# Kernel optimization log

Hardware: AMD Instinct MI355X
Metric: run time of the kernel (lower is better)

The kernel has to match this reference:

```python
import jax, jax.numpy as jnp
import numpy as np

NUM_ENT = 50000
N = 4 * NUM_ENT          # concat of id/gender/age/level embeds along dim 0
D = 128                  # init_dim = gcn_dim = embed_dim
H = 4                    # k_kernel attention heads
E = 600000
NUM_REL = 10
B = 4096


def _seg_softmax(scores, seg, n):
    # scores: [E, H], softmax over edges sharing the same destination node
    m = jax.ops.segment_max(scores, seg, num_segments=n)
    m = jnp.where(jnp.isfinite(m), m, 0.0)
    e = jnp.exp(scores - m[seg])
    s = jax.ops.segment_sum(e, seg, num_segments=n)
    return e / (s[seg] + 1e-16)


def _rgat_conv(x, rel_emb, src, dst, edge_type, W, W_rel, att):
    # CompGCN-style relational message (x_src + r_et) @ W, GAT-style attention,
    # per-destination segment softmax, scatter-sum aggregate, tanh activation.
    n = x.shape[0]
    xW = x @ W                        # [N, D_out]
    rW = rel_emb @ W                  # relation embed in message space
    d_out = xW.shape[1]
    dh = d_out // H
    m = (xW[src] + rW[edge_type]).reshape(-1, H, dh)   # [E, H, dh] messages
    q = xW[dst].reshape(-1, H, dh)                     # [E, H, dh] dest feats
    score = jax.nn.leaky_relu(
        (q * att[:, :dh]).sum(-1) + (m * att[:, dh:]).sum(-1), 0.2)  # [E, H]
    alpha = _seg_softmax(score, dst, n)                # [E, H]
    out = jax.ops.segment_sum((alpha[..., None] * m).reshape(-1, d_out), dst,
                              num_segments=n)          # [N, D_out]
    return jnp.tanh(out), rel_emb @ W_rel


def setup_inputs() -> dict:
    key = jax.random.key(0)
    ks = jax.random.split(key, 16)
    s = 0.1  # weight scale for numerical sanity
    return {
        "sub": jax.random.randint(ks[0], (B,), 0, N),
        "rel": jax.random.randint(ks[1], (B,), 0, 2 * NUM_REL),
        "edge_index": jax.random.randint(ks[2], (2, E), 0, N),
        "edge_type": jax.random.randint(ks[3], (E,), 0, 2 * NUM_REL),
        "ent_feature": jax.random.randint(ks[4], (NUM_ENT, 3), 0, 8),
        "gender_weight": s * jax.random.normal(ks[5], (8, D), jnp.float32),
        "age_weight": s * jax.random.normal(ks[6], (8, D), jnp.float32),
        "level_weight": s * jax.random.normal(ks[7], (8, D), jnp.float32),
        "id_embed": s * jax.random.normal(ks[8], (NUM_ENT, D), jnp.float32),
        "init_rel": s * jax.random.normal(ks[9], (2 * NUM_REL, D), jnp.float32),
        "W1": s * jax.random.normal(ks[10], (D, D), jnp.float32),
        "Wr1": s * jax.random.normal(ks[11], (D, D), jnp.float32),
        "att1": s * jax.random.normal(ks[12], (H, 2 * (D // H)), jnp.float32),
        "W2": s * jax.random.normal(ks[13], (D, D), jnp.float32),
        "Wr2": s * jax.random.normal(ks[14], (D, D), jnp.float32),
        "att2": s * jax.random.normal(ks[15], (H, 2 * (D // H)), jnp.float32),
    }


def reference(sub, rel, edge_index, edge_type, ent_feature,
              gender_weight, age_weight, level_weight, id_embed, init_rel,
              W1, Wr1, att1, W2, Wr2, att2):
    # feature embedding gathers + concat along node axis (as in __init__)
    gender_embed = gender_weight[ent_feature[:, 0]]
    age_embed = age_weight[ent_feature[:, 1]]
    level_embed = level_weight[ent_feature[:, 2]]
    x = jnp.concatenate([id_embed, gender_embed, age_embed, level_embed], axis=0)  # [N, D]
    src, dst = edge_index[0], edge_index[1]
    r = init_rel
    x, r = _rgat_conv(x, r, src, dst, edge_type, W1, Wr1, att1)
    # dropout modules run as identity (eval mode)
    x, r = _rgat_conv(x, r, src, dst, edge_type, W2, Wr2, att2)
    sub_emb = x[sub]
    rel_emb = r[rel]
    return (sub_emb, rel_emb, x)
```

## Files before the change

kernel.cpp:

```cpp
#include <hip/hip_runtime.h>

#define D 128
#define HEADS 4

typedef __attribute__((ext_vector_type(8))) short short8;
typedef __attribute__((ext_vector_type(4))) float f32x4;

__device__ __forceinline__ short f2b(float f) {
    unsigned u = __float_as_uint(f);
    unsigned r = (u + 0x7FFFu + ((u >> 16) & 1u)) >> 16;
    return (short)r;
}

__global__ __launch_bounds__(256) void gemm_mfma(
    const unsigned short* __restrict__ Ab, const short* __restrict__ Wt,
    unsigned short* __restrict__ C, const float* __restrict__ att,
    float* __restrict__ ns, int buildmode,
    const int* __restrict__ ent_feature, const float* __restrict__ gw,
    const float* __restrict__ aw, const float* __restrict__ lw,
    const float* __restrict__ idemb, int num_ent)
{
    __shared__ short sA[64 * D];
    __shared__ short sW[D * D];

    const int t = threadIdx.x;
    const long row0 = (long)blockIdx.x * 64;

    {
        int srow = t >> 2;
        int q = t & 3;
        long grow = row0 + srow;
        if (buildmode == 2) {
            const short8* p8 = (const short8*)(Ab + grow * D);
            #pragma unroll
            for (int jb = 0; jb < 4; ++jb) {
                short8 blk = p8[q * 4 + jb];
                int kb = (q * 4 + jb) ^ (srow & 7);
                *(short8*)&sA[srow * D + kb * 8] = blk;
            }
        } else {
            const float* srcp;
            if (grow < num_ent)               srcp = idemb + grow * D;
            else if (grow < 2L * num_ent)     srcp = gw + (long)ent_feature[(grow - num_ent) * 3 + 0] * D;
            else if (grow < 3L * num_ent)     srcp = aw + (long)ent_feature[(grow - 2L * num_ent) * 3 + 1] * D;
            else                              srcp = lw + (long)ent_feature[(grow - 3L * num_ent) * 3 + 2] * D;
            const float4* p4 = (const float4*)srcp + q * 8;
            float v[32];
            #pragma unroll
            for (int j = 0; j < 8; ++j) {
                float4 f = p4[j];
                v[j * 4 + 0] = f.x; v[j * 4 + 1] = f.y; v[j * 4 + 2] = f.z; v[j * 4 + 3] = f.w;
            }
            #pragma unroll
            for (int jb = 0; jb < 4; ++jb) {
                short8 blk;
                #pragma unroll
                for (int e = 0; e < 8; ++e) blk[e] = f2b(v[jb * 8 + e]);
                int kb = (q * 4 + jb) ^ (srow & 7);
                *(short8*)&sA[srow * D + kb * 8] = blk;
            }
        }
    }

    {
        #pragma unroll
        for (int i = 0; i < 8; ++i) {
            int c = t + 256 * i;
            int row = c >> 4, kb = c & 15;
            short8 blk = *(const short8*)(Wt + c * 8);
            *(short8*)&sW[row * D + (kb ^ (row & 7)) * 8] = blk;
        }
    }
    __syncthreads();

    const int wv = t >> 6, lane = t & 63;
    const int cl = lane & 15, kg = lane >> 4;

    short8 a[4];
    #pragma unroll
    for (int ks = 0; ks < 4; ++ks)
        a[ks] = *(const short8*)&sA[(wv * 16 + cl) * D + (((ks * 4 + kg) ^ (cl & 7)) * 8)];

    f32x4 acc[8];
    #pragma unroll
    for (int ct = 0; ct < 8; ++ct) acc[ct] = (f32x4){0.f, 0.f, 0.f, 0.f};

    #pragma unroll
    for (int ct = 0; ct < 8; ++ct) {
        #pragma unroll
        for (int ks = 0; ks < 4; ++ks) {
            short8 b = *(const short8*)&sW[(ct * 16 + cl) * D + (((ks * 4 + kg) ^ (cl & 7)) * 8)];
            acc[ct] = __builtin_amdgcn_mfma_f32_16x16x32_bf16(a[ks], b, acc[ct], 0, 0, 0);
        }
    }

    unsigned short* Cp = C + (row0 + wv * 16 + kg * 4) * D;
    #pragma unroll
    for (int ct = 0; ct < 8; ++ct)
        #pragma unroll
        for (int j = 0; j < 4; ++j)
            Cp[j * D + ct * 16 + cl] = (unsigned short)f2b(acc[ct][j]);

    float aqc[8], amc[8];
    #pragma unroll
    for (int ct = 0; ct < 8; ++ct) {
        int h = ct >> 1, cc = (ct & 1) * 16 + cl;
        aqc[ct] = att[h * 64 + cc];
        amc[ct] = att[h * 64 + 32 + cc];
    }
    float* scr = (float*)sA + wv * 1024;
    #pragma unroll
    for (int pass = 0; pass < 2; ++pass) {
        __syncthreads();
        #pragma unroll
        for (int jj = 0; jj < 2; ++jj) {
            int j = pass * 2 + jj;
            f32x4 lo, hi;
            #pragma unroll
            for (int h = 0; h < 4; ++h) {
                float qv = acc[2 * h][j] * aqc[2 * h] + acc[2 * h + 1][j] * aqc[2 * h + 1];
                float sv = acc[2 * h][j] * amc[2 * h] + acc[2 * h + 1][j] * amc[2 * h + 1];
                if (h < 2) { lo[h * 2] = qv; lo[h * 2 + 1] = sv; }
                else       { hi[(h - 2) * 2] = qv; hi[(h - 2) * 2 + 1] = sv; }
            }
            int base = ((kg * 16 + cl) * 2 + jj) * 8;
            *(f32x4*)&scr[base] = lo;
            *(f32x4*)&scr[base + 4] = hi;
        }
        __syncthreads();
        int kgr = lane >> 4, rem = lane & 15;
        int jjr = rem >> 3, hr = (rem >> 1) & 3, tr = rem & 1;
        float ssum = 0.f;
        #pragma unroll
        for (int c = 0; c < 16; ++c)
            ssum += scr[((kgr * 16 + c) * 2 + jjr) * 8 + hr * 2 + tr];
        long rown = row0 + wv * 16 + kgr * 4 + pass * 2 + jjr;
        ns[rown * 8 + tr * 4 + hr] = ssum;
    }
}

__global__ void prep1(const float* __restrict__ init_rel,
                      const float* __restrict__ W1, const float* __restrict__ Wr1,
                      const float* __restrict__ W2, const float* __restrict__ att1,
                      float* __restrict__ rWb, float* __restrict__ r1,
                      float* __restrict__ srt,
                      short* __restrict__ Wt1, short* __restrict__ Wt2, int nrel)
{
    __shared__ float red[128];
    int b = blockIdx.x, c = threadIdx.x;
    if (b >= 2 * nrel) {
        int bb = b - 2 * nrel;
        const float* W = (bb < D) ? W1 : W2;
        short* Wt = (bb < D) ? Wt1 : Wt2;
        int n = bb & (D - 1);
        Wt[n * D + c] = f2b(W[c * D + n]);
        return;
    }
    int r = (b < nrel) ? b : b - nrel;
    const float* W = (b < nrel) ? W1 : Wr1;
    float* out = (b < nrel) ? rWb : r1;
    float s = 0.f;
    for (int k = 0; k < D; ++k) s = fmaf(init_rel[r * D + k], W[k * D + c], s);
    out[r * D + c] = s;
    if (b < nrel) {
        int h = c >> 5;
        red[c] = s * att1[h * 64 + 32 + (c & 31)];
        __syncthreads();
        if (c < 4) {
            float ss = 0.f;
            #pragma unroll
            for (int k = 0; k < 32; ++k) ss += red[c * 32 + k];
            srt[r * 4 + c] = ss;
        }
    }
}

__global__ void prep2(const float* __restrict__ r1,
                      const float* __restrict__ W2, const float* __restrict__ Wr2,
                      const float* __restrict__ att2,
                      float* __restrict__ rWb, float* __restrict__ r2,
                      float* __restrict__ srt, int nrel)
{
    __shared__ float red[128];
    int b = blockIdx.x, c = threadIdx.x;
    int r = (b < nrel) ? b : b - nrel;
    const float* W = (b < nrel) ? W2 : Wr2;
    float* out = (b < nrel) ? rWb : r2;
    float s = 0.f;
    for (int k = 0; k < D; ++k) s = fmaf(r1[r * D + k], W[k * D + c], s);
    out[r * D + c] = s;
    if (b < nrel) {
        int h = c >> 5;
        red[c] = s * att2[h * 64 + 32 + (c & 31)];
        __syncthreads();
        if (c < 4) {
            float ss = 0.f;
            #pragma unroll
            for (int k = 0; k < 32; ++k) ss += red[c * 32 + k];
            srt[r * 4 + c] = ss;
        }
    }
}

__global__ __launch_bounds__(256) void hist_deg(const int* __restrict__ dst,
                                                int* __restrict__ deg, int E_)
{
    int i = blockIdx.x * 256 + threadIdx.x;
    if (i < E_) atomicAdd(&deg[dst[i]], 1);
}

__global__ __launch_bounds__(256) void scan_local(const int* __restrict__ deg,
                                                  int* __restrict__ offs,
                                                  int* __restrict__ partial, int n)
{
    __shared__ int lds[256];
    int b = blockIdx.x, t = threadIdx.x;
    int base = b * 1024;
    int v[4]; int s = 0;
    #pragma unroll
    for (int j = 0; j < 4; ++j) {
        int idx = base + t * 4 + j;
        v[j] = idx < n ? deg[idx] : 0;
        s += v[j];
    }
    lds[t] = s;
    __syncthreads();
    int mysum = s;
    for (int off = 1; off < 256; off <<= 1) {
        int o = t >= off ? lds[t - off] : 0;
        __syncthreads();
        lds[t] += o;
        __syncthreads();
    }
    int excl = lds[t] - mysum;
    if (t == 255) partial[b] = lds[255];
    int run = excl;
    #pragma unroll
    for (int j = 0; j < 4; ++j) {
        int idx = base + t * 4 + j;
        if (idx < n) offs[idx] = run;
        run += v[j];
    }
}

__global__ void scan_partials(int* __restrict__ partial, int nb, int* __restrict__ offs, int n)
{
    if (threadIdx.x == 0 && blockIdx.x == 0) {
        int run = 0;
        for (int i = 0; i < nb; ++i) { int v = partial[i]; partial[i] = run; run += v; }
        offs[n] = run;
    }
}

__global__ __launch_bounds__(256) void scan_add(int* __restrict__ offs,
                                                const int* __restrict__ partial, int n)
{
    int idx = blockIdx.x * 256 + threadIdx.x;
    if (idx < n) offs[idx] += partial[idx >> 10];
}

__global__ __launch_bounds__(256) void scatter_edges(
    const int* __restrict__ src, const int* __restrict__ dst, const int* __restrict__ etype,
    const int* __restrict__ offs, int* __restrict__ deg,
    int* __restrict__ sorted, int E_)
{
    int i = blockIdx.x * 256 + threadIdx.x;
    if (i >= E_) return;
    int d = dst[i];
    int pos = offs[d] + atomicSub(&deg[d], 1) - 1;
    sorted[pos] = src[i] | (etype[i] << 18);
}

#define GATHER_SLOT(mb, sv, rv, sr, p, cond)                              \
    unsigned mb = 0; float sv = 0.f, sr = 0.f; float2 rv = {0.f, 0.f};    \
    if (cond) { int s_ = (p) & 0x3FFFF, t_ = (p) >> 18;                   \
        mb = *(const unsigned*)(xWb + (long)s_ * D + 2 * lane);           \
        sv = ns[(long)s_ * 8 + 4 + h];                                    \
        rv = *(const float2*)(rW + (long)t_ * D + 2 * lane);              \
        sr = srt[t_ * 4 + h]; }

#define ACCUM_SLOT(mb, sv, rv, sr, qd, srun, ax, ay, cond)                \
    if (cond) { float mx = __uint_as_float(mb << 16) + rv.x;              \
        float my = __uint_as_float(mb & 0xFFFF0000u) + rv.y;              \
        float sc = qd + sv + sr; sc = sc > 0.f ? sc : 0.2f * sc;          \
        float we = __expf(sc);                                            \
        srun += we; ax = fmaf(we, mx, ax); ay = fmaf(we, my, ay); }

__global__ __launch_bounds__(256) void agg_node(
    const int* __restrict__ offs, const int* __restrict__ sedge,
    const unsigned short* __restrict__ xWb, const float* __restrict__ rW,
    const float* __restrict__ ns, const float* __restrict__ srt,
    void* __restrict__ outx, int out_bf16, int Nn)
{
    int wid = threadIdx.x >> 6;
    int lane = threadIdx.x & 63;
    long nA = (long)blockIdx.x * 8 + wid * 2;
    if (nA >= Nn) return;
    bool hasB = (nA + 1 < Nn);
    int h = lane >> 4;

    float qdA = ns[nA * 8 + h];
    float qdB = hasB ? ns[(nA + 1) * 8 + h] : 0.f;

    int2 oA = *(const int2*)&offs[nA];
    int e0A = oA.x, e1A = oA.y;
    int e0B = e1A, e1B = hasB ? offs[nA + 2] : e1A;

    float srunA = 0.f, axA = 0.f, ayA = 0.f;
    float srunB = 0.f, axB = 0.f, ayB = 0.f;

    int iA = e0A, iB = e0B;
    while (iA < e1A || iB < e1B) {
        int pA0 = (iA     < e1A) ? sedge[iA]     : 0;
        int pA1 = (iA + 1 < e1A) ? sedge[iA + 1] : 0;
        int pA2 = (iA + 2 < e1A) ? sedge[iA + 2] : 0;
        int pA3 = (iA + 3 < e1A) ? sedge[iA + 3] : 0;
        int pB0 = (iB     < e1B) ? sedge[iB]     : 0;
        int pB1 = (iB + 1 < e1B) ? sedge[iB + 1] : 0;
        int pB2 = (iB + 2 < e1B) ? sedge[iB + 2] : 0;
        int pB3 = (iB + 3 < e1B) ? sedge[iB + 3] : 0;

        GATHER_SLOT(mA0, vA0, rA0, sA0, pA0, iA     < e1A)
        GATHER_SLOT(mA1, vA1, rA1, sA1, pA1, iA + 1 < e1A)
        GATHER_SLOT(mA2, vA2, rA2, sA2, pA2, iA + 2 < e1A)
        GATHER_SLOT(mA3, vA3, rA3, sA3, pA3, iA + 3 < e1A)
        GATHER_SLOT(mB0, vB0, rB0, sB0, pB0, iB     < e1B)
        GATHER_SLOT(mB1, vB1, rB1, sB1, pB1, iB + 1 < e1B)
        GATHER_SLOT(mB2, vB2, rB2, sB2, pB2, iB + 2 < e1B)
        GATHER_SLOT(mB3, vB3, rB3, sB3, pB3, iB + 3 < e1B)

        ACCUM_SLOT(mA0, vA0, rA0, sA0, qdA, srunA, axA, ayA, iA     < e1A)
        ACCUM_SLOT(mA1, vA1, rA1, sA1, qdA, srunA, axA, ayA, iA + 1 < e1A)
        ACCUM_SLOT(mA2, vA2, rA2, sA2, qdA, srunA, axA, ayA, iA + 2 < e1A)
        ACCUM_SLOT(mA3, vA3, rA3, sA3, qdA, srunA, axA, ayA, iA + 3 < e1A)
        ACCUM_SLOT(mB0, vB0, rB0, sB0, qdB, srunB, axB, ayB, iB     < e1B)
        ACCUM_SLOT(mB1, vB1, rB1, sB1, qdB, srunB, axB, ayB, iB + 1 < e1B)
        ACCUM_SLOT(mB2, vB2, rB2, sB2, qdB, srunB, axB, ayB, iB + 2 < e1B)
        ACCUM_SLOT(mB3, vB3, rB3, sB3, qdB, srunB, axB, ayB, iB + 3 < e1B)

        iA += 4; iB += 4;
    }

    {
        float inv = 1.0f / (srunA + 1e-16f);
        float ox = tanhf(axA * inv);
        float oy = tanhf(ayA * inv);
        if (out_bf16) {
            unsigned pk = ((unsigned)(unsigned short)f2b(oy) << 16) | (unsigned short)f2b(ox);
            *(unsigned*)((unsigned short*)outx + nA * D + 2 * lane) = pk;
        } else {
            float2 o; o.x = ox; o.y = oy;
            *(float2*)((float*)outx + nA * D + 2 * lane) = o;
        }
    }
    if (hasB) {
        float inv = 1.0f / (srunB + 1e-16f);
        float ox = tanhf(axB * inv);
        float oy = tanhf(ayB * inv);
        if (out_bf16) {
            unsigned pk = ((unsigned)(unsigned short)f2b(oy) << 16) | (unsigned short)f2b(ox);
            *(unsigned*)((unsigned short*)outx + (nA + 1) * D + 2 * lane) = pk;
        } else {
            float2 o; o.x = ox; o.y = oy;
            *(float2*)((float*)outx + (nA + 1) * D + 2 * lane) = o;
        }
    }
}

__global__ void gather_out(const int* __restrict__ sub, const int* __restrict__ rel,
                           const float* __restrict__ xsrc, const float* __restrict__ rsrc,
                           float* __restrict__ out_sub, float* __restrict__ out_rel, int b)
{
    long i = (long)blockIdx.x * 256 + threadIdx.x;
    long tot = (long)b * 32;
    if (i < tot) {
        long row = i >> 5; int q = (int)(i & 31);
        ((float4*)out_sub)[i] = ((const float4*)(xsrc + (long)sub[row] * D))[q];
    } else if (i < 2 * tot) {
        long j = i - tot;
        long row = j >> 5; int q = (int)(j & 31);
        ((float4*)out_rel)[j] = ((const float4*)(rsrc + (long)rel[row] * D))[q];
    }
}

extern "C" void kernel_launch(void* const* d_in, const int* in_sizes, int n_in,
                              void* d_out, int out_size, void* d_ws, size_t ws_size,
                              hipStream_t stream)
{
    const int*   sub        = (const int*)d_in[0];
    const int*   rel        = (const int*)d_in[1];
    const int*   edge_index = (const int*)d_in[2];
    const int*   edge_type  = (const int*)d_in[3];
    const int*   ent_feat   = (const int*)d_in[4];
    const float* gw         = (const float*)d_in[5];
    const float* aw         = (const float*)d_in[6];
    const float* lw         = (const float*)d_in[7];
    const float* idemb      = (const float*)d_in[8];
    const float* init_rel   = (const float*)d_in[9];
    const float* W1         = (const float*)d_in[10];
    const float* Wr1        = (const float*)d_in[11];
    const float* att1       = (const float*)d_in[12];
    const float* W2         = (const float*)d_in[13];
    const float* Wr2        = (const float*)d_in[14];
    const float* att2       = (const float*)d_in[15];

    const int  Bn      = in_sizes[0];
    const int  E_      = in_sizes[3];
    const int  num_ent = in_sizes[4] / 3;
    const long Nn      = 4L * num_ent;
    const int  nrel    = in_sizes[9] / D;

    const int* srcp = edge_index;
    const int* dstp = edge_index + E_;

    float* out_sub = (float*)d_out;
    float* out_rel = out_sub + (long)Bn * D;
    float* out_x   = out_rel + (long)Bn * D;

    unsigned short* xWb = (unsigned short*)d_ws;
    unsigned short* x1b = xWb + Nn * D;
    int*   offs   = (int*)(x1b + Nn * D);
    int*   deg    = offs + (Nn + 1);
    int*   sorted = deg + Nn;
    int*   partial= sorted + E_;
    float* rWb    = (float*)(partial + 1024);
    float* r1     = rWb + (long)nrel * D;
    float* r2     = r1 + (long)nrel * D;
    short* Wt1    = (short*)(r2 + (long)nrel * D);
    short* Wt2    = Wt1 + D * D;
    float* ns     = (float*)(Wt2 + D * D);
    float* srt    = ns + Nn * 8;

    dim3 blk(256);
    int gemm_blocks  = (int)(Nn / 64);
    int e_blocks     = (E_ + 255) / 256;
    int agg_blocks   = (int)((Nn + 7) / 8);
    int gat_blocks   = (int)((2L * Bn * 32 + 255) / 256);
    int scan_blocks  = (int)((Nn + 1023) / 1024);
    int sadd_blocks  = (int)((Nn + 255) / 256);

    prep1<<<2 * nrel + 256, D, 0, stream>>>(init_rel, W1, Wr1, W2, att1,
                                            rWb, r1, srt, Wt1, Wt2, nrel);

    hipMemsetAsync(deg, 0, Nn * sizeof(int), stream);
    hist_deg<<<e_blocks, blk, 0, stream>>>(dstp, deg, E_);
    scan_local<<<scan_blocks, blk, 0, stream>>>(deg, offs, partial, (int)Nn);
    scan_partials<<<1, 64, 0, stream>>>(partial, scan_blocks, offs, (int)Nn);
    scan_add<<<sadd_blocks, blk, 0, stream>>>(offs, partial, (int)Nn);
    scatter_edges<<<e_blocks, blk, 0, stream>>>(srcp, dstp, edge_type, offs, deg, sorted, E_);

    gemm_mfma<<<gemm_blocks, blk, 0, stream>>>(nullptr, Wt1, xWb, att1, ns, 1,
                                               ent_feat, gw, aw, lw, idemb, num_ent);
    agg_node<<<agg_blocks, blk, 0, stream>>>(offs, sorted, xWb, rWb, ns, srt, x1b, 1, (int)Nn);

    prep2<<<2 * nrel, D, 0, stream>>>(r1, W2, Wr2, att2, rWb, r2, srt, nrel);
    gemm_mfma<<<gemm_blocks, blk, 0, stream>>>(x1b, Wt2, xWb, att2, ns, 2,
                                               nullptr, nullptr, nullptr, nullptr, nullptr, num_ent);
    agg_node<<<agg_blocks, blk, 0, stream>>>(offs, sorted, xWb, rWb, ns, srt, out_x, 0, (int)Nn);

    gather_out<<<gat_blocks, blk, 0, stream>>>(sub, rel, out_x, r2, out_sub, out_rel, Bn);
}
```

Measured before the change: 306.8 us.

## Store relation messages as bf16 and simplify aggregation to one node per wave

The per-relation message table rW is now stored as bf16 instead of fp32. Edges are packed as (src<<8)|etype so gather addresses come from byte offsets with fewer index multiplies. The aggregation kernel drops the two-nodes-per-wave interleave and processes one node per wave with 4-edge unrolling, launching twice as many blocks. This cuts per-edge load bytes and address arithmetic, but gives up the extra memory-level parallelism of interleaving two nodes and rounds relation embeddings to bf16.

```diff
diff --git a/kernel.cpp b/kernel.cpp
--- a/kernel.cpp
+++ b/kernel.cpp
@@ -142,7 +142,7 @@
 __global__ void prep1(const float* __restrict__ init_rel,
                       const float* __restrict__ W1, const float* __restrict__ Wr1,
                       const float* __restrict__ W2, const float* __restrict__ att1,
-                      float* __restrict__ rWb, float* __restrict__ r1,
+                      unsigned short* __restrict__ rw16, float* __restrict__ r1,
                       float* __restrict__ srt,
                       short* __restrict__ Wt1, short* __restrict__ Wt2, int nrel)
 {
@@ -158,11 +158,10 @@
     }
     int r = (b < nrel) ? b : b - nrel;
     const float* W = (b < nrel) ? W1 : Wr1;
-    float* out = (b < nrel) ? rWb : r1;
     float s = 0.f;
     for (int k = 0; k < D; ++k) s = fmaf(init_rel[r * D + k], W[k * D + c], s);
-    out[r * D + c] = s;
     if (b < nrel) {
+        rw16[r * D + c] = (unsigned short)f2b(s);
         int h = c >> 5;
         red[c] = s * att1[h * 64 + 32 + (c & 31)];
         __syncthreads();
@@ -172,24 +171,25 @@
             for (int k = 0; k < 32; ++k) ss += red[c * 32 + k];
             srt[r * 4 + c] = ss;
         }
+    } else {
+        r1[r * D + c] = s;
     }
 }
 
 __global__ void prep2(const float* __restrict__ r1,
                       const float* __restrict__ W2, const float* __restrict__ Wr2,
                       const float* __restrict__ att2,
-                      float* __restrict__ rWb, float* __restrict__ r2,
+                      unsigned short* __restrict__ rw16, float* __restrict__ r2,
                       float* __restrict__ srt, int nrel)
 {
     __shared__ float red[128];
     int b = blockIdx.x, c = threadIdx.x;
     int r = (b < nrel) ? b : b - nrel;
     const float* W = (b < nrel) ? W2 : Wr2;
-    float* out = (b < nrel) ? rWb : r2;
     float s = 0.f;
     for (int k = 0; k < D; ++k) s = fmaf(r1[r * D + k], W[k * D + c], s);
-    out[r * D + c] = s;
     if (b < nrel) {
+        rw16[r * D + c] = (unsigned short)f2b(s);
         int h = c >> 5;
         red[c] = s * att2[h * 64 + 32 + (c & 31)];
         __syncthreads();
@@ -199,6 +199,8 @@
             for (int k = 0; k < 32; ++k) ss += red[c * 32 + k];
             srt[r * 4 + c] = ss;
         }
+    } else {
+        r2[r * D + c] = s;
     }
 }
 
@@ -262,108 +264,81 @@
 __global__ __launch_bounds__(256) void scatter_edges(
     const int* __restrict__ src, const int* __restrict__ dst, const int* __restrict__ etype,
     const int* __restrict__ offs, int* __restrict__ deg,
-    int* __restrict__ sorted, int E_)
+    unsigned* __restrict__ sorted, int E_)
 {
     int i = blockIdx.x * 256 + threadIdx.x;
     if (i >= E_) return;
     int d = dst[i];
     int pos = offs[d] + atomicSub(&deg[d], 1) - 1;
-    sorted[pos] = src[i] | (etype[i] << 18);
-}
-
-#define GATHER_SLOT(mb, sv, rv, sr, p, cond)                              \
-    unsigned mb = 0; float sv = 0.f, sr = 0.f; float2 rv = {0.f, 0.f};    \
-    if (cond) { int s_ = (p) & 0x3FFFF, t_ = (p) >> 18;                   \
-        mb = *(const unsigned*)(xWb + (long)s_ * D + 2 * lane);           \
-        sv = ns[(long)s_ * 8 + 4 + h];                                    \
-        rv = *(const float2*)(rW + (long)t_ * D + 2 * lane);              \
-        sr = srt[t_ * 4 + h]; }
-
-#define ACCUM_SLOT(mb, sv, rv, sr, qd, srun, ax, ay, cond)                \
-    if (cond) { float mx = __uint_as_float(mb << 16) + rv.x;              \
-        float my = __uint_as_float(mb & 0xFFFF0000u) + rv.y;              \
-        float sc = qd + sv + sr; sc = sc > 0.f ? sc : 0.2f * sc;          \
-        float we = __expf(sc);                                            \
+    sorted[pos] = ((unsigned)src[i] << 8) | (unsigned)etype[i];
+}
+
+#define GATHER_SLOT(mb, sv, rv, sr, p, cond)                                 \
+    unsigned mb = 0, rv = 0; float sv = 0.f, sr = 0.f;                       \
+    if (cond) { unsigned rowb = (p) & 0xFFFFFF00u;                           \
+        unsigned etb = ((p) & 0xFFu) << 8;                                   \
+        mb = *(const unsigned*)(xb + rowb + lo4);                            \
+        sv = *(const float*)(nb + (rowb >> 3) + ho4);                        \
+        rv = *(const unsigned*)(rb + etb + lo4);                             \
+        sr = *(const float*)(sb + (etb >> 4) + (ho4 - 16)); }
+
+#define ACCUM_SLOT(mb, sv, rv, sr, cond)                                     \
+    if (cond) {                                                              \
+        float mx = __uint_as_float(mb << 16) + __uint_as_float(rv << 16);    \
+        float my = __uint_as_float(mb & 0xFFFF0000u) + __uint_as_float(rv & 0xFFFF0000u); \
+        float sc = qd + sv + sr; sc = sc > 0.f ? sc : 0.2f * sc;             \
+        float we = __expf(sc);                                               \
         srun += we; ax = fmaf(we, mx, ax); ay = fmaf(we, my, ay); }
 
 __global__ __launch_bounds__(256) void agg_node(
-    const int* __restrict__ offs, const int* __restrict__ sedge,
-    const unsigned short* __restrict__ xWb, const float* __restrict__ rW,
+    const int* __restrict__ offs, const unsigned* __restrict__ sedge,
+    const unsigned short* __restrict__ xWb, const unsigned short* __restrict__ rw16,
     const float* __restrict__ ns, const float* __restrict__ srt,
     void* __restrict__ outx, int out_bf16, int Nn)
 {
     int wid = threadIdx.x >> 6;
     int lane = threadIdx.x & 63;
-    long nA = (long)blockIdx.x * 8 + wid * 2;
-    if (nA >= Nn) return;
-    bool hasB = (nA + 1 < Nn);
+    long node = (long)blockIdx.x * 4 + wid;
+    if (node >= Nn) return;
     int h = lane >> 4;
 
-    float qdA = ns[nA * 8 + h];
-    float qdB = hasB ? ns[(nA + 1) * 8 + h] : 0.f;
-
-    int2 oA = *(const int2*)&offs[nA];
-    int e0A = oA.x, e1A = oA.y;
-    int e0B = e1A, e1B = hasB ? offs[nA + 2] : e1A;
-
-    float srunA = 0.f, axA = 0.f, ayA = 0.f;
-    float srunB = 0.f, axB = 0.f, ayB = 0.f;
-
-    int iA = e0A, iB = e0B;
-    while (iA < e1A || iB < e1B) {
-        int pA0 = (iA     < e1A) ? sedge[iA]     : 0;
-        int pA1 = (iA + 1 < e1A) ? sedge[iA + 1] : 0;
-        int pA2 = (iA + 2 < e1A) ? sedge[iA + 2] : 0;
-        int pA3 = (iA + 3 < e1A) ? sedge[iA + 3] : 0;
-        int pB0 = (iB     < e1B) ? sedge[iB]     : 0;
-        int pB1 = (iB + 1 < e1B) ? sedge[iB + 1] : 0;
-        int pB2 = (iB + 2 < e1B) ? sedge[iB + 2] : 0;
-        int pB3 = (iB + 3 < e1B) ? sedge[iB + 3] : 0;
-
-        GATHER_SLOT(mA0, vA0, rA0, sA0, pA0, iA     < e1A)
-        GATHER_SLOT(mA1, vA1, rA1, sA1, pA1, iA + 1 < e1A)
-        GATHER_SLOT(mA2, vA2, rA2, sA2, pA2, iA + 2 < e1A)
-        GATHER_SLOT(mA3, vA3, rA3, sA3, pA3, iA + 3 < e1A)
-        GATHER_SLOT(mB0, vB0, rB0, sB0, pB0, iB     < e1B)
-        GATHER_SLOT(mB1, vB1, rB1, sB1, pB1, iB + 1 < e1B)
-        GATHER_SLOT(mB2, vB2, rB2, sB2, pB2, iB + 2 < e1B)
-        GATHER_SLOT(mB3, vB3, rB3, sB3, pB3, iB + 3 < e1B)
-
-        ACCUM_SLOT(mA0, vA0, rA0, sA0, qdA, srunA, axA, ayA, iA     < e1A)
-        ACCUM_SLOT(mA1, vA1, rA1, sA1, qdA, srunA, axA, ayA, iA + 1 < e1A)
-        ACCUM_SLOT(mA2, vA2, rA2, sA2, qdA, srunA, axA, ayA, iA + 2 < e1A)
-        ACCUM_SLOT(mA3, vA3, rA3, sA3, qdA, srunA, axA, ayA, iA + 3 < e1A)
-        ACCUM_SLOT(mB0, vB0, rB0, sB0, qdB, srunB, axB, ayB, iB     < e1B)
-        ACCUM_SLOT(mB1, vB1, rB1, sB1, qdB, srunB, axB, ayB, iB + 1 < e1B)
-        ACCUM_SLOT(mB2, vB2, rB2, sB2, qdB, srunB, axB, ayB, iB + 2 < e1B)
-        ACCUM_SLOT(mB3, vB3, rB3, sB3, qdB, srunB, axB, ayB, iB + 3 < e1B)
-
-        iA += 4; iB += 4;
-    }
-
-    {
-        float inv = 1.0f / (srunA + 1e-16f);
-        float ox = tanhf(axA * inv);
-        float oy = tanhf(ayA * inv);
-        if (out_bf16) {
-            unsigned pk = ((unsigned)(unsigned short)f2b(oy) << 16) | (unsigned short)f2b(ox);
-            *(unsigned*)((unsigned short*)outx + nA * D + 2 * lane) = pk;
-        } else {
-            float2 o; o.x = ox; o.y = oy;
-            *(float2*)((float*)outx + nA * D + 2 * lane) = o;
-        }
-    }
-    if (hasB) {
-        float inv = 1.0f / (srunB + 1e-16f);
-        float ox = tanhf(axB * inv);
-        float oy = tanhf(ayB * inv);
-        if (out_bf16) {
-            unsigned pk = ((unsigned)(unsigned short)f2b(oy) << 16) | (unsigned short)f2b(ox);
-            *(unsigned*)((unsigned short*)outx + (nA + 1) * D + 2 * lane) = pk;
-        } else {
-            float2 o; o.x = ox; o.y = oy;
-            *(float2*)((float*)outx + (nA + 1) * D + 2 * lane) = o;
-        }
+    const char* xb = (const char*)xWb;
+    const char* rb = (const char*)rw16;
+    const char* nb = (const char*)ns;
+    const char* sb = (const char*)srt;
+    const int lo4 = 4 * lane;
+    const int ho4 = 16 + 4 * h;
+
+    float qd = ns[node * 8 + h];
+    int e0 = offs[node], e1 = offs[node + 1];
+    float srun = 0.f, ax = 0.f, ay = 0.f;
+
+    for (int base = e0; base < e1; base += 4) {
+        unsigned p0 = sedge[base];
+        unsigned p1 = (base + 1 < e1) ? sedge[base + 1] : 0;
+        unsigned p2 = (base + 2 < e1) ? sedge[base + 2] : 0;
+        unsigned p3 = (base + 3 < e1) ? sedge[base + 3] : 0;
+
+        GATHER_SLOT(m0, v0, r0, s0, p0, true)
+        GATHER_SLOT(m1, v1, r1, s1, p1, base + 1 < e1)
+        GATHER_SLOT(m2, v2, r2, s2, p2, base + 2 < e1)
+        GATHER_SLOT(m3, v3, r3, s3, p3, base + 3 < e1)
+
+        ACCUM_SLOT(m0, v0, r0, s0, true)
+        ACCUM_SLOT(m1, v1, r1, s1, base + 1 < e1)
+        ACCUM_SLOT(m2, v2, r2, s2, base + 2 < e1)
+        ACCUM_SLOT(m3, v3, r3, s3, base + 3 < e1)
+    }
+
+    float inv = 1.0f / (srun + 1e-16f);
+    float ox = tanhf(ax * inv);
+    float oy = tanhf(ay * inv);
+    if (out_bf16) {
+        unsigned pk = ((unsigned)(unsigned short)f2b(oy) << 16) | (unsigned short)f2b(ox);
+        *(unsigned*)((unsigned short*)outx + node * D + 2 * lane) = pk;
+    } else {
+        float2 o; o.x = ox; o.y = oy;
+        *(float2*)((float*)outx + node * D + 2 * lane) = o;
     }
 }
 
@@ -419,12 +394,12 @@
 
     unsigned short* xWb = (unsigned short*)d_ws;
     unsigned short* x1b = xWb + Nn * D;
-    int*   offs   = (int*)(x1b + Nn * D);
-    int*   deg    = offs + (Nn + 1);
-    int*   sorted = deg + Nn;
-    int*   partial= sorted + E_;
-    float* rWb    = (float*)(partial + 1024);
-    float* r1     = rWb + (long)nrel * D;
+    int*      offs   = (int*)(x1b + Nn * D);
+    int*      deg    = offs + (Nn + 1);
+    unsigned* sorted = (unsigned*)(deg + Nn);
+    int*      partial= (int*)(sorted + E_);
+    unsigned short* rw16 = (unsigned short*)(partial + 1024);
+    float* r1     = (float*)(rw16 + (long)nrel * D);
     float* r2     = r1 + (long)nrel * D;
     short* Wt1    = (short*)(r2 + (long)nrel * D);
     short* Wt2    = Wt1 + D * D;
@@ -434,13 +409,13 @@
     dim3 blk(256);
     int gemm_blocks  = (int)(Nn / 64);
     int e_blocks     = (E_ + 255) / 256;
-    int agg_blocks   = (int)((Nn + 7) / 8);
+    int agg_blocks   = (int)((Nn + 3) / 4);
     int gat_blocks   = (int)((2L * Bn * 32 + 255) / 256);
     int scan_blocks  = (int)((Nn + 1023) / 1024);
     int sadd_blocks  = (int)((Nn + 255) / 256);
 
     prep1<<<2 * nrel + 256, D, 0, stream>>>(init_rel, W1, Wr1, W2, att1,
-                                            rWb, r1, srt, Wt1, Wt2, nrel);
+                                            rw16, r1, srt, Wt1, Wt2, nrel);
 
     hipMemsetAsync(deg, 0, Nn * sizeof(int), stream);
     hist_deg<<<e_blocks, blk, 0, stream>>>(dstp, deg, E_);
@@ -451,12 +426,12 @@
 
     gemm_mfma<<<gemm_blocks, blk, 0, stream>>>(nullptr, Wt1, xWb, att1, ns, 1,
                                                ent_feat, gw, aw, lw, idemb, num_ent);
-    agg_node<<<agg_blocks, blk, 0, stream>>>(offs, sorted, xWb, rWb, ns, srt, x1b, 1, (int)Nn);
-
-    prep2<<<2 * nrel, D, 0, stream>>>(r1, W2, Wr2, att2, rWb, r2, srt, nrel);
+    agg_node<<<agg_blocks, blk, 0, stream>>>(offs, sorted, xWb, rw16, ns, srt, x1b, 1, (int)Nn);
+
+    prep2<<<2 * nrel, D, 0, stream>>>(r1, W2, Wr2, att2, rw16, r2, srt, nrel);
     gemm_mfma<<<gemm_blocks, blk, 0, stream>>>(x1b, Wt2, xWb, att2, ns, 2,
                                                nullptr, nullptr, nullptr, nullptr, nullptr, num_ent);
-    agg_node<<<agg_blocks, blk, 0, stream>>>(offs, sorted, xWb, rWb, ns, srt, out_x, 0, (int)Nn);
+    agg_node<<<agg_blocks, blk, 0, stream>>>(offs, sorted, xWb, rw16, ns, srt, out_x, 0, (int)Nn);
 
     gather_out<<<gat_blocks, blk, 0, stream>>>(sub, rel, out_x, r2, out_sub, out_rel, Bn);
 }
```

Result: faster. 300.0 us (-2.2%).
